# Optimization experiments

Measured on AMD Instinct MI355X. Metric: run time of the kernel, lower is better.

## Reference

```python
import jax, jax.numpy as jnp
import numpy as np

N_NODES = 50000
N_EDGES = 1000000
NODE_F = 64
EDGE_F = 64
OUT_F = 128
K = 2  # matches init k=2


def setup_inputs() -> dict:
    key = jax.random.key(0)
    k1, k2, k3, k4, k5, k6 = jax.random.split(key, 6)
    node_feat = jax.random.normal(k1, (N_NODES, NODE_F), dtype=jnp.float32)
    edge_feat = jax.random.normal(k2, (N_EDGES, EDGE_F), dtype=jnp.float32)
    # nn.Linear(edge_feats*2 + node_feats, out_feats): weight [out, in], bias [out]
    W = jax.random.normal(k3, (OUT_F, 2 * EDGE_F + NODE_F), dtype=jnp.float32) * 0.05
    b = jax.random.normal(k4, (OUT_F,), dtype=jnp.float32) * 0.05
    src = jax.random.randint(k5, (N_EDGES,), 0, N_NODES, dtype=jnp.int64)
    dst = jax.random.randint(k6, (N_EDGES,), 0, N_NODES, dtype=jnp.int64)
    return {"node_feat": node_feat, "edge_feat": edge_feat, "W": W, "b": b,
            "src": src, "dst": dst}


def reference(node_feat, edge_feat, W, b, src, dst):
    N = node_feat.shape[0]
    # norm = in_degrees().clamp(min=1) ** -0.5, shape [N, 1]
    deg = jax.ops.segment_sum(jnp.ones_like(dst, dtype=node_feat.dtype), dst,
                              num_segments=N)
    norm = jnp.maximum(deg, 1.0) ** -0.5
    norm = norm[:, None]
    # DGL semantics: update_all(copy_e, sum) overwrites ndata['h'] with the
    # scatter-sum of edge data over destination nodes; apply_edges then copies
    # the (un-normalized) node 'h' back to edges via edge.src.
    e = edge_feat  # [E, EDGE_F]
    fstack = [node_feat]
    for _ in range(K):
        h = jax.ops.segment_sum(e, dst, num_segments=N)  # [N, EDGE_F]
        fstack.append(h * norm)
        e = h[src]  # apply_edges: e = src node h (un-normalized)
    rst = jnp.concatenate(fstack, axis=-1) @ W.T + b  # [N, OUT_F]
    est = rst[src]  # final apply_edges copies lin output to edges
    return rst, est
```

## Files before the change

kernel.cpp:

```cpp
#include <hip/hip_runtime.h>
#include <hip/hip_bf16.h>

#define NF 64
#define N_OUT 128
#define CAT 192
#define CAPL 6
#define CAP 64

typedef __attribute__((ext_vector_type(4))) float f32x4;
typedef __attribute__((ext_vector_type(8))) short bf16x8;

__device__ inline unsigned short f2bf(float x) {
  unsigned u = __float_as_uint(x);
  unsigned r = (u + 0x7fff + ((u >> 16) & 1)) >> 16;
  return (unsigned short)r;
}

__device__ inline ushort4 pack4(f32x4 v) {
  ushort4 r;
  r.x = f2bf(v.x); r.y = f2bf(v.y); r.z = f2bf(v.z); r.w = f2bf(v.w);
  return r;
}

__device__ inline f32x4 unpack4(ushort4 b) {
  f32x4 v;
  v.x = __uint_as_float((unsigned)b.x << 16);
  v.y = __uint_as_float((unsigned)b.y << 16);
  v.z = __uint_as_float((unsigned)b.z << 16);
  v.w = __uint_as_float((unsigned)b.w << 16);
  return v;
}

__device__ inline f32x4 sx4(f32x4 v, int m) {
  f32x4 r;
  r.x = __shfl_xor(v.x, m, 64);
  r.y = __shfl_xor(v.y, m, 64);
  r.z = __shfl_xor(v.z, m, 64);
  r.w = __shfl_xor(v.w, m, 64);
  return r;
}

__global__ __launch_bounds__(256) void fill_kernel(const int* __restrict__ src,
                                                   const int* __restrict__ dst,
                                                   int* __restrict__ cnt,
                                                   long long* __restrict__ bins,
                                                   int n_edges) {
  int i = blockIdx.x * blockDim.x + threadIdx.x;
  if (i >= n_edges) return;
  int d = __builtin_nontemporal_load(&dst[i]);
  int s = __builtin_nontemporal_load(&src[i]);
  int p = atomicAdd(&cnt[d], 1) & (CAP - 1);
  long long pk = (long long)(((unsigned long long)(unsigned)s << 32) | (unsigned)i);
  bins[((size_t)d << CAPL) + p] = pk;
}

__global__ __launch_bounds__(256) void h1_kernel(const float* __restrict__ edge_feat,
                                                 const float* __restrict__ node_feat,
                                                 const int2* __restrict__ bins,
                                                 const int* __restrict__ cnt,
                                                 unsigned short* __restrict__ h1r,
                                                 unsigned short* __restrict__ h1n,
                                                 unsigned short* __restrict__ nfb,
                                                 int n_nodes) {
  int n = blockIdx.x * 4 + (threadIdx.x >> 6);
  if (n >= n_nodes) return;
  int l = threadIdx.x & 63;
  int l15 = l & 15, l4 = l >> 4;
  int c = cnt[n];
  if (c > CAP) c = CAP;
  int kb = n << CAPL;
  int ke = kb + c;
  f32x4 acc0 = {0.f,0.f,0.f,0.f}, acc1 = {0.f,0.f,0.f,0.f};
  f32x4 acc2 = {0.f,0.f,0.f,0.f}, acc3 = {0.f,0.f,0.f,0.f};
  int k = kb;
  for (; k + 16 <= ke; k += 16) {
    int e0 = bins[k + l4].x;
    int e1 = bins[k + 4 + l4].x;
    int e2 = bins[k + 8 + l4].x;
    int e3 = bins[k + 12 + l4].x;
    acc0 += __builtin_nontemporal_load((const f32x4*)&edge_feat[(size_t)e0 * NF + l15 * 4]);
    acc1 += __builtin_nontemporal_load((const f32x4*)&edge_feat[(size_t)e1 * NF + l15 * 4]);
    acc2 += __builtin_nontemporal_load((const f32x4*)&edge_feat[(size_t)e2 * NF + l15 * 4]);
    acc3 += __builtin_nontemporal_load((const f32x4*)&edge_feat[(size_t)e3 * NF + l15 * 4]);
  }
  if (k + 8 <= ke) {
    int e0 = bins[k + l4].x;
    int e1 = bins[k + 4 + l4].x;
    acc0 += __builtin_nontemporal_load((const f32x4*)&edge_feat[(size_t)e0 * NF + l15 * 4]);
    acc1 += __builtin_nontemporal_load((const f32x4*)&edge_feat[(size_t)e1 * NF + l15 * 4]);
    k += 8;
  }
  if (k + 4 <= ke) {
    int e = bins[k + l4].x;
    acc2 += __builtin_nontemporal_load((const f32x4*)&edge_feat[(size_t)e * NF + l15 * 4]);
    k += 4;
  }
  int rem = ke - k;
  if (l4 < rem) {
    int e = bins[k + l4].x;
    acc3 += __builtin_nontemporal_load((const f32x4*)&edge_feat[(size_t)e * NF + l15 * 4]);
  }
  f32x4 t = (acc0 + acc1) + (acc2 + acc3);
  t += sx4(t, 16);
  t += sx4(t, 32);
  if (l4 == 0) {
    *(ushort4*)&h1r[(size_t)n * NF + l15 * 4] = pack4(t);
    float nm = rsqrtf(fmaxf((float)c, 1.0f));
    f32x4 tn = t; tn.x *= nm; tn.y *= nm; tn.z *= nm; tn.w *= nm;
    *(ushort4*)&h1n[(size_t)n * NF + l15 * 4] = pack4(tn);
  } else if (l4 == 1) {
    f32x4 v = *(const f32x4*)&node_feat[(size_t)n * NF + l15 * 4];
    *(ushort4*)&nfb[(size_t)n * NF + l15 * 4] = pack4(v);
  }
}

__global__ __launch_bounds__(256) void h2_kernel(const unsigned short* __restrict__ h1r,
                                                 const int2* __restrict__ bins,
                                                 const int* __restrict__ cnt,
                                                 unsigned short* __restrict__ h2n,
                                                 int n_nodes) {
  int n = blockIdx.x * 4 + (threadIdx.x >> 6);
  if (n >= n_nodes) return;
  int l = threadIdx.x & 63;
  int l15 = l & 15, l4 = l >> 4;
  int c = cnt[n];
  if (c > CAP) c = CAP;
  int kb = n << CAPL;
  int ke = kb + c;
  f32x4 acc0 = {0.f,0.f,0.f,0.f}, acc1 = {0.f,0.f,0.f,0.f};
  f32x4 acc2 = {0.f,0.f,0.f,0.f}, acc3 = {0.f,0.f,0.f,0.f};
  int k = kb;
  for (; k + 16 <= ke; k += 16) {
    int s0 = bins[k + l4].y;
    int s1 = bins[k + 4 + l4].y;
    int s2 = bins[k + 8 + l4].y;
    int s3 = bins[k + 12 + l4].y;
    acc0 += unpack4(*(const ushort4*)&h1r[(size_t)s0 * NF + l15 * 4]);
    acc1 += unpack4(*(const ushort4*)&h1r[(size_t)s1 * NF + l15 * 4]);
    acc2 += unpack4(*(const ushort4*)&h1r[(size_t)s2 * NF + l15 * 4]);
    acc3 += unpack4(*(const ushort4*)&h1r[(size_t)s3 * NF + l15 * 4]);
  }
  if (k + 8 <= ke) {
    int s0 = bins[k + l4].y;
    int s1 = bins[k + 4 + l4].y;
    acc0 += unpack4(*(const ushort4*)&h1r[(size_t)s0 * NF + l15 * 4]);
    acc1 += unpack4(*(const ushort4*)&h1r[(size_t)s1 * NF + l15 * 4]);
    k += 8;
  }
  if (k + 4 <= ke) {
    int s = bins[k + l4].y;
    acc2 += unpack4(*(const ushort4*)&h1r[(size_t)s * NF + l15 * 4]);
    k += 4;
  }
  int rem = ke - k;
  if (l4 < rem) {
    int s = bins[k + l4].y;
    acc3 += unpack4(*(const ushort4*)&h1r[(size_t)s * NF + l15 * 4]);
  }
  f32x4 t = (acc0 + acc1) + (acc2 + acc3);
  t += sx4(t, 16);
  t += sx4(t, 32);
  if (l4 == 0) {
    float nm = rsqrtf(fmaxf((float)c, 1.0f));
    t.x *= nm; t.y *= nm; t.z *= nm; t.w *= nm;
    *(ushort4*)&h2n[(size_t)n * NF + l15 * 4] = pack4(t);
  }
}

__global__ __launch_bounds__(512) void gemm_kernel(const unsigned short* __restrict__ nfb,
                                                   const unsigned short* __restrict__ h1n,
                                                   const unsigned short* __restrict__ h2n,
                                                   const float* __restrict__ W,
                                                   const float* __restrict__ bias,
                                                   float* __restrict__ rst,
                                                   unsigned short* __restrict__ rstb,
                                                   int n_nodes) {
  __shared__ short F[64 * 200];
  __shared__ float R[64][132];
  int tid = threadIdx.x;
  int l = tid & 63, w = tid >> 6;
  int w2 = w & 3, wh = w >> 2;
  int l15 = l & 15, l4 = l >> 4;

  bf16x8 Bf[6][2];
  #pragma unroll
  for (int c = 0; c < 2; ++c) {
    int col = w2 * 32 + c * 16 + l15;
    const float* wp = &W[(size_t)col * CAT];
    #pragma unroll
    for (int ks = 0; ks < 6; ++ks) {
      int k0 = ks * 32 + l4 * 8;
      bf16x8 b;
      #pragma unroll
      for (int j = 0; j < 8; ++j) b[j] = (short)f2bf(wp[k0 + j]);
      Bf[ks][c] = b;
    }
  }
  float bias0 = bias[w2 * 32 + l15];
  float bias1 = bias[w2 * 32 + 16 + l15];

  int tiles = (n_nodes + 63) / 64;
  for (int tile = blockIdx.x; tile < tiles; tile += gridDim.x) {
    int nbase = tile * 64;
    __syncthreads();
    for (int idx = tid; idx < 1536; idx += 512) {
      int m = idx / 24, q = idx - m * 24;
      int n = nbase + m;
      bf16x8 pk = bf16x8{0,0,0,0,0,0,0,0};
      if (n < n_nodes) {
        const unsigned short* base = (q < 8) ? nfb : (q < 16) ? h1n : h2n;
        pk = *(const bf16x8*)&base[(size_t)n * NF + (q & 7) * 8];
      }
      *(bf16x8*)&F[m * 200 + q * 8] = pk;
    }
    __syncthreads();
    f32x4 acc00 = {0.f,0.f,0.f,0.f}, acc01 = {0.f,0.f,0.f,0.f};
    f32x4 acc10 = {0.f,0.f,0.f,0.f}, acc11 = {0.f,0.f,0.f,0.f};
    #pragma unroll
    for (int ks = 0; ks < 6; ++ks) {
      bf16x8 a0 = *(const bf16x8*)&F[(wh * 32 + l15) * 200 + ks * 32 + l4 * 8];
      bf16x8 a1 = *(const bf16x8*)&F[(wh * 32 + 16 + l15) * 200 + ks * 32 + l4 * 8];
      acc00 = __builtin_amdgcn_mfma_f32_16x16x32_bf16(a0, Bf[ks][0], acc00, 0, 0, 0);
      acc01 = __builtin_amdgcn_mfma_f32_16x16x32_bf16(a0, Bf[ks][1], acc01, 0, 0, 0);
      acc10 = __builtin_amdgcn_mfma_f32_16x16x32_bf16(a1, Bf[ks][0], acc10, 0, 0, 0);
      acc11 = __builtin_amdgcn_mfma_f32_16x16x32_bf16(a1, Bf[ks][1], acc11, 0, 0, 0);
    }
    #pragma unroll
    for (int rt = 0; rt < 2; ++rt) {
      f32x4 ac0 = rt ? acc10 : acc00;
      f32x4 ac1 = rt ? acc11 : acc01;
      #pragma unroll
      for (int r = 0; r < 4; ++r) {
        int row = wh * 32 + rt * 16 + l4 * 4 + r;
        R[row][w2 * 32 + l15] = ac0[r] + bias0;
        R[row][w2 * 32 + 16 + l15] = ac1[r] + bias1;
      }
    }
    __syncthreads();
    for (int idx = tid; idx < 64 * 32; idx += 512) {
      int m = idx >> 5, c = idx & 31;
      int n = nbase + m;
      if (n < n_nodes) {
        f32x4 v = *(const f32x4*)&R[m][c * 4];
        __builtin_nontemporal_store(v, (f32x4*)&rst[(size_t)n * N_OUT + c * 4]);
      }
    }
    for (int idx = tid; idx < 64 * 16; idx += 512) {
      int m = idx >> 4, q = idx & 15;
      int n = nbase + m;
      if (n < n_nodes) {
        const float* rp = &R[m][q * 8];
        bf16x8 pk;
        #pragma unroll
        for (int j = 0; j < 8; ++j) pk[j] = (short)f2bf(rp[j]);
        *(bf16x8*)&rstb[(size_t)n * N_OUT + q * 8] = pk;
      }
    }
  }
}

__global__ __launch_bounds__(256) void est_bf16_kernel(const unsigned short* __restrict__ rstb,
                                                       const int* __restrict__ src,
                                                       float* __restrict__ est, int n_edges) {
  f32x4* e4 = (f32x4*)est;
  int total = n_edges * 32;
  int i = blockIdx.x * blockDim.x + threadIdx.x;
  int stride = gridDim.x * blockDim.x;
  for (; i < total; i += stride) {
    int e = i >> 5, c = i & 31;
    ushort4 b = *(const ushort4*)&rstb[(size_t)src[e] * N_OUT + c * 4];
    __builtin_nontemporal_store(unpack4(b), &e4[i]);
  }
}

extern "C" void kernel_launch(void* const* d_in, const int* in_sizes, int n_in,
                              void* d_out, int out_size, void* d_ws, size_t ws_size,
                              hipStream_t stream) {
  const float* node_feat = (const float*)d_in[0];
  const float* edge_feat = (const float*)d_in[1];
  const float* W = (const float*)d_in[2];
  const float* bias = (const float*)d_in[3];
  const int* src = (const int*)d_in[4];
  const int* dst = (const int*)d_in[5];
  int n_nodes = in_sizes[0] / NF;
  int n_edges = in_sizes[4];

  size_t off = 0;
  auto take = [&](size_t bytes) -> void* {
    void* p = (char*)d_ws + off;
    off += (bytes + 255) & ~(size_t)255;
    return p;
  };
  int* cnt = (int*)take((size_t)n_nodes * 4);
  long long* bins = (long long*)take((size_t)n_nodes * CAP * 8);
  unsigned short* h1r = (unsigned short*)take((size_t)n_nodes * NF * 2);
  unsigned short* h1n = (unsigned short*)take((size_t)n_nodes * NF * 2);
  unsigned short* h2n = (unsigned short*)take((size_t)n_nodes * NF * 2);
  unsigned short* nfb = (unsigned short*)take((size_t)n_nodes * NF * 2);
  unsigned short* rstb = (unsigned short*)take((size_t)n_nodes * N_OUT * 2);

  float* rst = (float*)d_out;
  float* est = rst + (size_t)n_nodes * N_OUT;

  (void)hipMemsetAsync(cnt, 0, (size_t)n_nodes * 4, stream);

  fill_kernel<<<(n_edges + 255) / 256, 256, 0, stream>>>(src, dst, cnt, bins, n_edges);
  int nb = (n_nodes + 3) / 4;
  h1_kernel<<<nb, 256, 0, stream>>>(edge_feat, node_feat, (const int2*)bins, cnt,
                                    h1r, h1n, nfb, n_nodes);
  h2_kernel<<<nb, 256, 0, stream>>>(h1r, (const int2*)bins, cnt, h2n, n_nodes);
  gemm_kernel<<<512, 512, 0, stream>>>(nfb, h1n, h2n, W, bias, rst, rstb, n_nodes);
  est_bf16_kernel<<<8192, 256, 0, stream>>>(rstb, src, est, n_edges);
}
```

Baseline: 321.5 us.

## Widen est copy per thread, enlarge fill blocks, loop gather tails

The est expansion kernel now has each thread handle 8 output columns, with two 8-byte loads and two 16-byte nontemporal stores, which halves the number of index lookups and loop iterations. The fill kernel is launched with 1024-thread blocks instead of 256. The tail handling in the h1 and h2 gather kernels is replaced by a 4-edge loop that rotates through the accumulators. The accumulators become an array indexed by a runtime value, which may push them to scratch memory or add selects.

```diff
diff --git a/kernel.cpp b/kernel.cpp
--- a/kernel.cpp
+++ b/kernel.cpp
@@ -40,11 +40,11 @@
   return r;
 }
 
-__global__ __launch_bounds__(256) void fill_kernel(const int* __restrict__ src,
-                                                   const int* __restrict__ dst,
-                                                   int* __restrict__ cnt,
-                                                   long long* __restrict__ bins,
-                                                   int n_edges) {
+__global__ __launch_bounds__(1024) void fill_kernel(const int* __restrict__ src,
+                                                    const int* __restrict__ dst,
+                                                    int* __restrict__ cnt,
+                                                    long long* __restrict__ bins,
+                                                    int n_edges) {
   int i = blockIdx.x * blockDim.x + threadIdx.x;
   if (i >= n_edges) return;
   int d = __builtin_nontemporal_load(&dst[i]);
@@ -70,37 +70,31 @@
   if (c > CAP) c = CAP;
   int kb = n << CAPL;
   int ke = kb + c;
-  f32x4 acc0 = {0.f,0.f,0.f,0.f}, acc1 = {0.f,0.f,0.f,0.f};
-  f32x4 acc2 = {0.f,0.f,0.f,0.f}, acc3 = {0.f,0.f,0.f,0.f};
+  f32x4 acc[4];
+  acc[0] = f32x4{0.f,0.f,0.f,0.f}; acc[1] = f32x4{0.f,0.f,0.f,0.f};
+  acc[2] = f32x4{0.f,0.f,0.f,0.f}; acc[3] = f32x4{0.f,0.f,0.f,0.f};
   int k = kb;
   for (; k + 16 <= ke; k += 16) {
     int e0 = bins[k + l4].x;
     int e1 = bins[k + 4 + l4].x;
     int e2 = bins[k + 8 + l4].x;
     int e3 = bins[k + 12 + l4].x;
-    acc0 += __builtin_nontemporal_load((const f32x4*)&edge_feat[(size_t)e0 * NF + l15 * 4]);
-    acc1 += __builtin_nontemporal_load((const f32x4*)&edge_feat[(size_t)e1 * NF + l15 * 4]);
-    acc2 += __builtin_nontemporal_load((const f32x4*)&edge_feat[(size_t)e2 * NF + l15 * 4]);
-    acc3 += __builtin_nontemporal_load((const f32x4*)&edge_feat[(size_t)e3 * NF + l15 * 4]);
-  }
-  if (k + 8 <= ke) {
-    int e0 = bins[k + l4].x;
-    int e1 = bins[k + 4 + l4].x;
-    acc0 += __builtin_nontemporal_load((const f32x4*)&edge_feat[(size_t)e0 * NF + l15 * 4]);
-    acc1 += __builtin_nontemporal_load((const f32x4*)&edge_feat[(size_t)e1 * NF + l15 * 4]);
-    k += 8;
-  }
-  if (k + 4 <= ke) {
+    acc[0] += __builtin_nontemporal_load((const f32x4*)&edge_feat[(size_t)e0 * NF + l15 * 4]);
+    acc[1] += __builtin_nontemporal_load((const f32x4*)&edge_feat[(size_t)e1 * NF + l15 * 4]);
+    acc[2] += __builtin_nontemporal_load((const f32x4*)&edge_feat[(size_t)e2 * NF + l15 * 4]);
+    acc[3] += __builtin_nontemporal_load((const f32x4*)&edge_feat[(size_t)e3 * NF + l15 * 4]);
+  }
+  int rot = 0;
+  for (; k + 4 <= ke; k += 4, ++rot) {
     int e = bins[k + l4].x;
-    acc2 += __builtin_nontemporal_load((const f32x4*)&edge_feat[(size_t)e * NF + l15 * 4]);
-    k += 4;
+    acc[rot & 3] += __builtin_nontemporal_load((const f32x4*)&edge_feat[(size_t)e * NF + l15 * 4]);
   }
   int rem = ke - k;
   if (l4 < rem) {
     int e = bins[k + l4].x;
-    acc3 += __builtin_nontemporal_load((const f32x4*)&edge_feat[(size_t)e * NF + l15 * 4]);
-  }
-  f32x4 t = (acc0 + acc1) + (acc2 + acc3);
+    acc[3] += __builtin_nontemporal_load((const f32x4*)&edge_feat[(size_t)e * NF + l15 * 4]);
+  }
+  f32x4 t = (acc[0] + acc[1]) + (acc[2] + acc[3]);
   t += sx4(t, 16);
   t += sx4(t, 32);
   if (l4 == 0) {
@@ -127,37 +121,31 @@
   if (c > CAP) c = CAP;
   int kb = n << CAPL;
   int ke = kb + c;
-  f32x4 acc0 = {0.f,0.f,0.f,0.f}, acc1 = {0.f,0.f,0.f,0.f};
-  f32x4 acc2 = {0.f,0.f,0.f,0.f}, acc3 = {0.f,0.f,0.f,0.f};
+  f32x4 acc[4];
+  acc[0] = f32x4{0.f,0.f,0.f,0.f}; acc[1] = f32x4{0.f,0.f,0.f,0.f};
+  acc[2] = f32x4{0.f,0.f,0.f,0.f}; acc[3] = f32x4{0.f,0.f,0.f,0.f};
   int k = kb;
   for (; k + 16 <= ke; k += 16) {
     int s0 = bins[k + l4].y;
     int s1 = bins[k + 4 + l4].y;
     int s2 = bins[k + 8 + l4].y;
     int s3 = bins[k + 12 + l4].y;
-    acc0 += unpack4(*(const ushort4*)&h1r[(size_t)s0 * NF + l15 * 4]);
-    acc1 += unpack4(*(const ushort4*)&h1r[(size_t)s1 * NF + l15 * 4]);
-    acc2 += unpack4(*(const ushort4*)&h1r[(size_t)s2 * NF + l15 * 4]);
-    acc3 += unpack4(*(const ushort4*)&h1r[(size_t)s3 * NF + l15 * 4]);
-  }
-  if (k + 8 <= ke) {
-    int s0 = bins[k + l4].y;
-    int s1 = bins[k + 4 + l4].y;
-    acc0 += unpack4(*(const ushort4*)&h1r[(size_t)s0 * NF + l15 * 4]);
-    acc1 += unpack4(*(const ushort4*)&h1r[(size_t)s1 * NF + l15 * 4]);
-    k += 8;
-  }
-  if (k + 4 <= ke) {
+    acc[0] += unpack4(*(const ushort4*)&h1r[(size_t)s0 * NF + l15 * 4]);
+    acc[1] += unpack4(*(const ushort4*)&h1r[(size_t)s1 * NF + l15 * 4]);
+    acc[2] += unpack4(*(const ushort4*)&h1r[(size_t)s2 * NF + l15 * 4]);
+    acc[3] += unpack4(*(const ushort4*)&h1r[(size_t)s3 * NF + l15 * 4]);
+  }
+  int rot = 0;
+  for (; k + 4 <= ke; k += 4, ++rot) {
     int s = bins[k + l4].y;
-    acc2 += unpack4(*(const ushort4*)&h1r[(size_t)s * NF + l15 * 4]);
-    k += 4;
+    acc[rot & 3] += unpack4(*(const ushort4*)&h1r[(size_t)s * NF + l15 * 4]);
   }
   int rem = ke - k;
   if (l4 < rem) {
     int s = bins[k + l4].y;
-    acc3 += unpack4(*(const ushort4*)&h1r[(size_t)s * NF + l15 * 4]);
-  }
-  f32x4 t = (acc0 + acc1) + (acc2 + acc3);
+    acc[3] += unpack4(*(const ushort4*)&h1r[(size_t)s * NF + l15 * 4]);
+  }
+  f32x4 t = (acc[0] + acc[1]) + (acc[2] + acc[3]);
   t += sx4(t, 16);
   t += sx4(t, 32);
   if (l4 == 0) {
@@ -263,13 +251,16 @@
                                                        const int* __restrict__ src,
                                                        float* __restrict__ est, int n_edges) {
   f32x4* e4 = (f32x4*)est;
-  int total = n_edges * 32;
+  int total = n_edges * 16;
   int i = blockIdx.x * blockDim.x + threadIdx.x;
   int stride = gridDim.x * blockDim.x;
   for (; i < total; i += stride) {
-    int e = i >> 5, c = i & 31;
-    ushort4 b = *(const ushort4*)&rstb[(size_t)src[e] * N_OUT + c * 4];
-    __builtin_nontemporal_store(unpack4(b), &e4[i]);
+    int e = i >> 4, c = i & 15;
+    const ushort4* rp = (const ushort4*)&rstb[(size_t)src[e] * N_OUT + c * 8];
+    ushort4 b0 = rp[0];
+    ushort4 b1 = rp[1];
+    __builtin_nontemporal_store(unpack4(b0), &e4[i * 2]);
+    __builtin_nontemporal_store(unpack4(b1), &e4[i * 2 + 1]);
   }
 }
 
@@ -304,7 +295,7 @@
 
   (void)hipMemsetAsync(cnt, 0, (size_t)n_nodes * 4, stream);
 
-  fill_kernel<<<(n_edges + 255) / 256, 256, 0, stream>>>(src, dst, cnt, bins, n_edges);
+  fill_kernel<<<(n_edges + 1023) / 1024, 1024, 0, stream>>>(src, dst, cnt, bins, n_edges);
   int nb = (n_nodes + 3) / 4;
   h1_kernel<<<nb, 256, 0, stream>>>(edge_feat, node_feat, (const int2*)bins, cnt,
                                     h1r, h1n, nfb, n_nodes);
```

After: 361.9 us. 1.13x slower.
